# Kernel optimization log

Hardware: AMD Instinct MI355X
Metric: run time of the kernel (lower is better)

Reference implementation:

```python
import jax, jax.numpy as jnp
import numpy as np

D = 3          # matrix dimension (fixed in source)
WIDTH = 23     # hidden channel width (fixed in source)
B = 524288     # batch of 3x3 symmetric matrices

# layer channel dims: {1:1}->{1:W}, W->W, W->W, W->1
_LAYER_DIMS = [(1, WIDTH), (WIDTH, WIDTH), (WIDTH, WIDTH), (WIDTH, 1)]


def setup_inputs() -> dict:
    key = jax.random.key(0)
    ks = jax.random.split(key, 1 + 3 * len(_LAYER_DIMS))
    a = jax.random.normal(ks[0], (B, D, D), dtype=jnp.float32)
    x = a + jnp.swapaxes(a, -1, -2)  # symmetric inputs, as eigh expects
    inp = {"x": x}
    for li, (ic, oc) in enumerate(_LAYER_DIMS):
        s = 1.0 / np.sqrt(2.0 * ic * D)
        inp[f"w_id{li}"] = (jax.random.normal(ks[1 + 3 * li], (oc, ic)) * s).astype(jnp.float32)
        inp[f"w_sum{li}"] = (jax.random.normal(ks[2 + 3 * li], (oc, ic)) * s).astype(jnp.float32)
        inp[f"b{li}"] = jnp.zeros((oc,), dtype=jnp.float32)
    return inp


def _perm_layer(t, w_id, w_sum, b):
    # t: (B, in_c, D). S_D-equivariant linear map on order-1 tensors:
    # identity basis + all-ones(sum) basis + constant-vector bias.
    y = jnp.einsum('oc,bcd->bod', w_id, t)
    y = y + jnp.einsum('oc,bc->bo', w_sum, t.sum(-1))[:, :, None]
    return y + b[None, :, None]


def reference(x, w_id0, w_sum0, b0, w_id1, w_sum1, b1,
              w_id2, w_sum2, b2, w_id3, w_sum3, b3):
    evals, evecs = jnp.linalg.eigh(x)          # (B,D), (B,D,D)
    t = evals[:, None, :]                      # (B,1,D)
    layers = [(w_id0, w_sum0, b0), (w_id1, w_sum1, b1),
              (w_id2, w_sum2, b2), (w_id3, w_sum3, b3)]
    for i, (wi, ws, b) in enumerate(layers):
        t = _perm_layer(t, wi, ws, b)
        if i < len(layers) - 1:
            t = jax.nn.relu(t)
    ev = t[:, 0, :]                            # (B,D) transformed eigenvalues
    # eigvecs @ diag(ev) @ eigvecs^T, batched
    return jnp.einsum('bik,bk,bjk->bij', evecs, ev, evecs)
```

## Files before the change

kernel.cpp:

```cpp
#include <hip/hip_runtime.h>
#include <math.h>


#define MLP_W 23

typedef _Float16 h2    __attribute__((ext_vector_type(2)));
typedef _Float16 f16x4 __attribute__((ext_vector_type(4)));
typedef _Float16 f16x8 __attribute__((ext_vector_type(8)));
typedef float    f32x4 __attribute__((ext_vector_type(4)));
typedef float    v2f   __attribute__((ext_vector_type(2)));
typedef float    f4a   __attribute__((ext_vector_type(4), aligned(4)));

__device__ __attribute__((aligned(16))) h2 g_afrag[2][2][2][64][4];
__device__ __attribute__((aligned(16))) h2 g_a3frag[64][4];
__device__ __attribute__((aligned(16))) float g_l0[3][24];

__global__ void svh_prep_kernel(const float* __restrict__ wi0, const float* __restrict__ ws0,
                                const float* __restrict__ b0,
                                const float* __restrict__ wi1, const float* __restrict__ ws1,
                                const float* __restrict__ wi2, const float* __restrict__ ws2,
                                const float* __restrict__ wi3, const float* __restrict__ ws3) {
    int t = blockIdx.x * blockDim.x + threadIdx.x;
    if (t < 512) {
        int lane  = t & 63;
        int mt    = (t >> 6) & 1;
        int mat   = (t >> 7) & 1;
        int layer = (t >> 8) & 1;
        const float* W = layer ? (mat ? ws2 : wi2) : (mat ? ws1 : wi1);
        int row = mt * 16 + (lane & 15);
        int g   = lane >> 4;
#pragma unroll
        for (int dw = 0; dw < 4; ++dw) {
            int k0 = 8 * g + 2 * dw, k1 = k0 + 1;
            float a = (row < MLP_W && k0 < MLP_W) ? W[row * MLP_W + k0] : 0.0f;
            float b = (row < MLP_W && k1 < MLP_W) ? W[row * MLP_W + k1] : 0.0f;
            g_afrag[layer][mat][mt][lane][dw] = (h2){(_Float16)a, (_Float16)b};
        }
    }
    if (t < 64) {
        int lane = t;
        int row  = lane & 15;
        int g    = lane >> 4;
#pragma unroll
        for (int dw = 0; dw < 4; ++dw) {
            int k0 = 8 * g + 2 * dw, k1 = k0 + 1;
            float a = 0.0f, b = 0.0f;
            if (row == 0) {
                a = (k0 < MLP_W) ? wi3[k0] : 0.0f;
                b = (k1 < MLP_W) ? wi3[k1] : 0.0f;
            } else if (row == 1) {
                a = (k0 < MLP_W) ? ws3[k0] : 0.0f;
                b = (k1 < MLP_W) ? ws3[k1] : 0.0f;
            }
            g_a3frag[lane][dw] = (h2){(_Float16)a, (_Float16)b};
        }
    }
    if (t < 24) {
        g_l0[0][t] = (t < MLP_W) ? wi0[t] : 0.0f;
        g_l0[1][t] = (t < MLP_W) ? ws0[t] : 0.0f;
        g_l0[2][t] = (t < MLP_W) ? b0[t]  : 0.0f;
    }
}

__device__ __forceinline__ float sinv(float d) {
    return (fabsf(d) > 1e-20f) ? (1.0f / d) : 0.0f;
}

__device__ __forceinline__ f32x4 mm16(f16x8 a, f16x8 b) {
    return __builtin_amdgcn_mfma_f32_16x16x32_f16(a, b, (f32x4){0.f, 0.f, 0.f, 0.f}, 0, 0, 0);
}
__device__ __forceinline__ f32x4 mm16a(f16x8 a, f16x8 b, f32x4 c) {
    return __builtin_amdgcn_mfma_f32_16x16x32_f16(a, b, c, 0, 0, 0);
}

#define COLB 144
#define ZOFF (64 * COLB)
#define LDSZ (ZOFF + 16)

__global__ __launch_bounds__(64, 4)
void svh_eig_mlp_kernel(
    const float* __restrict__ x,
    const float* __restrict__ bb1, const float* __restrict__ bb2, const float* __restrict__ bb3,
    float* __restrict__ out, int B)
{
    __shared__ alignas(16) unsigned char lds[LDSZ];

    const int lane = threadIdx.x;
    const int g    = lane >> 4;
    const int c16  = lane & 15;
    int idx  = blockIdx.x * 64 + lane;
    int cidx = (idx < B) ? idx : (B - 1);

    const float* xp = x + (size_t)cidx * 9;
    f4a xa = *(const f4a*)(xp);
    f4a xb = *(const f4a*)(xp + 4);
    float x22 = xp[8];
    float x00 = xa[0], x01 = xa[1], x02 = xa[2];
    float x11 = xb[0], x12 = xb[1];

    if (lane == 0) *(f32x4*)(lds + ZOFF) = (f32x4){0.f, 0.f, 0.f, 0.f};

    float q   = (x00 + x11 + x22) * (1.0f / 3.0f);
    float a00 = x00 - q, a11 = x11 - q, a22 = x22 - q;
    float p1  = x01 * x01 + x02 * x02 + x12 * x12;
    float p2  = a00 * a00 + a11 * a11 + a22 * a22 + 2.0f * p1;
    float p   = sqrtf(p2 * (1.0f / 6.0f));
    float ip  = sinv(p);
    float d00 = a00 * ip, d11 = a11 * ip, d22 = a22 * ip;
    float c01 = x01 * ip, c02 = x02 * ip, c12 = x12 * ip;
    float detB = d00 * (d11 * d22 - c12 * c12)
               - c01 * (c01 * d22 - c12 * c02)
               + c02 * (c01 * c12 - d11 * c02);
    float r = 0.5f * detB;
    r = fminf(1.0f, fmaxf(-1.0f, r));
    float phi  = acosf(r) * (1.0f / 3.0f);
    float cph  = __cosf(phi);
    float sph  = sqrtf(fmaxf(0.0f, 1.0f - cph * cph));
    const float SQ3 = 1.7320508075688772f;
    float lc = q + 2.0f * p * cph;
    float la = q - p * cph - SQ3 * p * sph;
    float lb = q - p * cph + SQ3 * p * sph;

    {
        float S = la + lb + lc;
        v2f Sv = {S, S}, lav = {la, la}, lbv = {lb, lb}, lcv = {lc, lc};
        v2f z2 = {0.f, 0.f};
        const v2f* L0WI = (const v2f*)g_l0[0];
        const v2f* L0WS = (const v2f*)g_l0[1];
        const v2f* L0BB = (const v2f*)g_l0[2];
        const int base = lane * COLB;
#pragma unroll
        for (int m = 0; m < 6; ++m) {
            v2f wiA = L0WI[2 * m], wiB = L0WI[2 * m + 1];
            v2f uA  = __builtin_elementwise_fma(L0WS[2 * m],     Sv, L0BB[2 * m]);
            v2f uB  = __builtin_elementwise_fma(L0WS[2 * m + 1], Sv, L0BB[2 * m + 1]);
            v2f a0 = __builtin_elementwise_max(__builtin_elementwise_fma(wiA, lav, uA), z2);
            v2f b0 = __builtin_elementwise_max(__builtin_elementwise_fma(wiB, lav, uB), z2);
            v2f a1 = __builtin_elementwise_max(__builtin_elementwise_fma(wiA, lbv, uA), z2);
            v2f b1 = __builtin_elementwise_max(__builtin_elementwise_fma(wiB, lbv, uB), z2);
            v2f a2 = __builtin_elementwise_max(__builtin_elementwise_fma(wiA, lcv, uA), z2);
            v2f b2 = __builtin_elementwise_max(__builtin_elementwise_fma(wiB, lcv, uB), z2);
            int cb = base + (m >> 1) * 48 + (m & 1) * 8;
            *(f16x4*)(lds + cb +  0) = (f16x4){(_Float16)a0.x, (_Float16)a0.y, (_Float16)b0.x, (_Float16)b0.y};
            *(f16x4*)(lds + cb + 16) = (f16x4){(_Float16)a1.x, (_Float16)a1.y, (_Float16)b1.x, (_Float16)b1.y};
            *(f16x4*)(lds + cb + 32) = (f16x4){(_Float16)a2.x, (_Float16)a2.y, (_Float16)b2.x, (_Float16)b2.y};
        }
    }

    const f16x8 A3 = *(const f16x8*)(&g_a3frag[lane][0]);

    float eva = 0.0f, evb = 0.0f, evc = 0.0f;
    const f32x4 z4 = {0.f, 0.f, 0.f, 0.f};

#pragma unroll
    for (int L = 0; L < 2; ++L) {
        f16x8 WiM0 = *(const f16x8*)(&g_afrag[L][0][0][lane][0]);
        f16x8 WiM1 = *(const f16x8*)(&g_afrag[L][0][1][lane][0]);
        f16x8 WsM0 = *(const f16x8*)(&g_afrag[L][1][0][lane][0]);
        f16x8 WsM1 = *(const f16x8*)(&g_afrag[L][1][1][lane][0]);
        const float* bb = L ? bb2 : bb1;
        f32x4 bvec[2];
#pragma unroll
        for (int mt = 0; mt < 2; ++mt)
#pragma unroll
            for (int rr = 0; rr < 4; ++rr) {
                int row = mt * 16 + 4 * g + rr;
                bvec[mt][rr] = (row < MLP_W) ? bb[row] : 0.0f;
            }

#pragma unroll
        for (int pp = 0; pp < 4; ++pp) {
            const int colb = (16 * pp + c16) * COLB;
            f16x8 bf[3];
#pragma unroll
            for (int h = 0; h < 3; ++h) {
                int off = (g == 3) ? ZOFF : (colb + g * 48 + h * 16);
                bf[h] = *(const f16x8*)(lds + off);
            }
            f32x4 c0m0 = mm16(WiM0, bf[0]);
            f32x4 c0m1 = mm16(WiM1, bf[0]);
            f32x4 c1m0 = mm16(WiM0, bf[1]);
            f32x4 c1m1 = mm16(WiM1, bf[1]);
            f32x4 c2m0 = mm16(WiM0, bf[2]);
            f32x4 c2m1 = mm16(WiM1, bf[2]);
            f32x4 sm0 = mm16a(WsM0, bf[2], mm16a(WsM0, bf[1], mm16(WsM0, bf[0])));
            f32x4 sm1 = mm16a(WsM1, bf[2], mm16a(WsM1, bf[1], mm16(WsM1, bf[0])));

#pragma unroll
            for (int mt = 0; mt < 2; ++mt) {
                if (mt == 1 && g >= 2) continue;
                f32x4 c0 = (mt == 0) ? c0m0 : c0m1;
                f32x4 c1 = (mt == 0) ? c1m0 : c1m1;
                f32x4 c2 = (mt == 0) ? c2m0 : c2m1;
                f32x4 cs = (mt == 0) ? sm0  : sm1;
                f32x4 u  = cs + bvec[mt];
                f32x4 y0 = __builtin_elementwise_max(c0 + u, z4);
                f32x4 y1 = __builtin_elementwise_max(c1 + u, z4);
                f32x4 y2 = __builtin_elementwise_max(c2 + u, z4);
                int wb = colb + (2 * mt + (g >> 1)) * 48 + (g & 1) * 8;
                *(f16x4*)(lds + wb +  0) = (f16x4){(_Float16)y0[0], (_Float16)y0[1], (_Float16)y0[2], (_Float16)y0[3]};
                *(f16x4*)(lds + wb + 16) = (f16x4){(_Float16)y1[0], (_Float16)y1[1], (_Float16)y1[2], (_Float16)y1[3]};
                *(f16x4*)(lds + wb + 32) = (f16x4){(_Float16)y2[0], (_Float16)y2[1], (_Float16)y2[2], (_Float16)y2[3]};
            }

            if (L == 1) {
                f16x8 b2f[3];
#pragma unroll
                for (int h = 0; h < 3; ++h) {
                    int off = (g == 3) ? ZOFF : (colb + g * 48 + h * 16);
                    b2f[h] = *(const f16x8*)(lds + off);
                }
                f32x4 D0 = mm16(A3, b2f[0]);
                f32x4 D1 = mm16(A3, b2f[1]);
                f32x4 D2 = mm16(A3, b2f[2]);
                float ssum = D0[1] + D1[1] + D2[1];
                float ea = D0[0] + ssum;
                float eb = D1[0] + ssum;
                float ec = D2[0] + ssum;
                ea = __shfl(ea, c16);
                eb = __shfl(eb, c16);
                ec = __shfl(ec, c16);
                bool own = (g == pp);
                eva = own ? ea : eva;
                evb = own ? eb : evb;
                evc = own ? ec : evc;
            }
        }
    }

    {
        float b3v = bb3[0];
        eva += b3v; evb += b3v; evc += b3v;
    }

    float g1 = (evb - eva) * sinv(lb - la);
    float g2 = (evc - evb) * sinv(lc - lb);
    float c2 = (g2 - g1) * sinv(lc - la);

    float m100 = x00 - la, m111 = x11 - la, m122 = x22 - la;
    float m200 = x00 - lb, m211 = x11 - lb, m222 = x22 - lb;

    float P00 = m100 * m200 + x01 * x01 + x02 * x02;
    float P01 = m100 * x01 + x01 * m211 + x02 * x12;
    float P02 = m100 * x02 + x01 * x12 + x02 * m222;
    float P11 = x01 * x01 + m111 * m211 + x12 * x12;
    float P12 = x01 * x02 + m111 * x12 + x12 * m222;
    float P22 = x02 * x02 + x12 * x12 + m122 * m222;

    float o00 = fmaf(g1, m100, eva) + c2 * P00;
    float o01 = g1 * x01 + c2 * P01;
    float o02 = g1 * x02 + c2 * P02;
    float o11 = fmaf(g1, m111, eva) + c2 * P11;
    float o12 = g1 * x12 + c2 * P12;
    float o22 = fmaf(g1, m122, eva) + c2 * P22;

    if (idx < B) {
        float* op = out + (size_t)idx * 9;
        op[0] = o00; op[1] = o01; op[2] = o02;
        op[3] = o01; op[4] = o11; op[5] = o12;
        op[6] = o02; op[7] = o12; op[8] = o22;
    }
}

extern "C" void kernel_launch(void* const* d_in, const int* in_sizes, int n_in,
                              void* d_out, int out_size, void* d_ws, size_t ws_size,
                              hipStream_t stream) {
    const float* x   = (const float*)d_in[0];
    const float* wi0 = (const float*)d_in[1];
    const float* ws0 = (const float*)d_in[2];
    const float* b0  = (const float*)d_in[3];
    const float* wi1 = (const float*)d_in[4];
    const float* ws1 = (const float*)d_in[5];
    const float* b1  = (const float*)d_in[6];
    const float* wi2 = (const float*)d_in[7];
    const float* ws2 = (const float*)d_in[8];
    const float* b2  = (const float*)d_in[9];
    const float* wi3 = (const float*)d_in[10];
    const float* ws3 = (const float*)d_in[11];
    const float* b3  = (const float*)d_in[12];

    int B = in_sizes[0] / 9;
    float* out = (float*)d_out;

    {
        dim3 block(256);
        dim3 grid(2);
        hipLaunchKernelGGL(svh_prep_kernel, grid, block, 0, stream,
                           wi0, ws0, b0, wi1, ws1, wi2, ws2, wi3, ws3);
    }

    dim3 block(64);
    dim3 grid((B + 63) / 64);
    hipLaunchKernelGGL(svh_eig_mlp_kernel, grid, block, 0, stream,
                       x, b1, b2, b3, out, B);
}
```

Before: 117.0 us.

## Fold layer biases into MFMA via ones channel, polynomial acos, vector stores

Folds the hidden-layer biases into the padded 24th input channel of the sum-weight fragments by setting that channel to 1 in the activations. This removes per-thread bias loads and adds. Also replaces acosf with a short minimax polynomial times a square root, and writes the output with two 16-byte-vector stores plus one scalar store instead of nine scalar stores. The bias now passes through fp16, which may cost some accuracy, and the polynomial acos is less precise.

```diff
diff --git a/kernel.cpp b/kernel.cpp
--- a/kernel.cpp
+++ b/kernel.cpp
@@ -18,7 +18,9 @@
 __global__ void svh_prep_kernel(const float* __restrict__ wi0, const float* __restrict__ ws0,
                                 const float* __restrict__ b0,
                                 const float* __restrict__ wi1, const float* __restrict__ ws1,
+                                const float* __restrict__ b1,
                                 const float* __restrict__ wi2, const float* __restrict__ ws2,
+                                const float* __restrict__ b2,
                                 const float* __restrict__ wi3, const float* __restrict__ ws3) {
     int t = blockIdx.x * blockDim.x + threadIdx.x;
     if (t < 512) {
@@ -26,7 +28,8 @@
         int mt    = (t >> 6) & 1;
         int mat   = (t >> 7) & 1;
         int layer = (t >> 8) & 1;
-        const float* W = layer ? (mat ? ws2 : wi2) : (mat ? ws1 : wi1);
+        const float* W  = layer ? (mat ? ws2 : wi2) : (mat ? ws1 : wi1);
+        const float* BI = layer ? b2 : b1;
         int row = mt * 16 + (lane & 15);
         int g   = lane >> 4;
 #pragma unroll
@@ -34,6 +37,7 @@
             int k0 = 8 * g + 2 * dw, k1 = k0 + 1;
             float a = (row < MLP_W && k0 < MLP_W) ? W[row * MLP_W + k0] : 0.0f;
             float b = (row < MLP_W && k1 < MLP_W) ? W[row * MLP_W + k1] : 0.0f;
+            if (mat == 1 && k1 == 23 && row < MLP_W) b = BI[row];
             g_afrag[layer][mat][mt][lane][dw] = (h2){(_Float16)a, (_Float16)b};
         }
     }
@@ -80,7 +84,7 @@
 __global__ __launch_bounds__(64, 4)
 void svh_eig_mlp_kernel(
     const float* __restrict__ x,
-    const float* __restrict__ bb1, const float* __restrict__ bb2, const float* __restrict__ bb3,
+    const float* __restrict__ bb3,
     float* __restrict__ out, int B)
 {
     __shared__ alignas(16) unsigned char lds[LDSZ];
@@ -113,7 +117,18 @@
                + c02 * (c01 * c12 - d11 * c02);
     float r = 0.5f * detB;
     r = fminf(1.0f, fmaxf(-1.0f, r));
-    float phi  = acosf(r) * (1.0f / 3.0f);
+    float ar  = fabsf(r);
+    float sq  = sqrtf(fmaxf(0.0f, 1.0f - ar));
+    float po  = fmaf(ar, -0.0012624911f, 0.0066700901f);
+    po = fmaf(ar, po, -0.0170881256f);
+    po = fmaf(ar, po,  0.0308918810f);
+    po = fmaf(ar, po, -0.0501743046f);
+    po = fmaf(ar, po,  0.0889789874f);
+    po = fmaf(ar, po, -0.2145988016f);
+    po = fmaf(ar, po,  1.5707963050f);
+    float acs = sq * po * (1.0f / 3.0f);
+    const float PI3 = 1.0471975511965976f;
+    float phi = (r >= 0.0f) ? acs : (PI3 - acs);
     float cph  = __cosf(phi);
     float sph  = sqrtf(fmaxf(0.0f, 1.0f - cph * cph));
     const float SQ3 = 1.7320508075688772f;
@@ -140,6 +155,7 @@
             v2f b1 = __builtin_elementwise_max(__builtin_elementwise_fma(wiB, lbv, uB), z2);
             v2f a2 = __builtin_elementwise_max(__builtin_elementwise_fma(wiA, lcv, uA), z2);
             v2f b2 = __builtin_elementwise_max(__builtin_elementwise_fma(wiB, lcv, uB), z2);
+            if (m == 5) b0.y = 1.0f;
             int cb = base + (m >> 1) * 48 + (m & 1) * 8;
             *(f16x4*)(lds + cb +  0) = (f16x4){(_Float16)a0.x, (_Float16)a0.y, (_Float16)b0.x, (_Float16)b0.y};
             *(f16x4*)(lds + cb + 16) = (f16x4){(_Float16)a1.x, (_Float16)a1.y, (_Float16)b1.x, (_Float16)b1.y};
@@ -158,15 +174,6 @@
         f16x8 WiM1 = *(const f16x8*)(&g_afrag[L][0][1][lane][0]);
         f16x8 WsM0 = *(const f16x8*)(&g_afrag[L][1][0][lane][0]);
         f16x8 WsM1 = *(const f16x8*)(&g_afrag[L][1][1][lane][0]);
-        const float* bb = L ? bb2 : bb1;
-        f32x4 bvec[2];
-#pragma unroll
-        for (int mt = 0; mt < 2; ++mt)
-#pragma unroll
-            for (int rr = 0; rr < 4; ++rr) {
-                int row = mt * 16 + 4 * g + rr;
-                bvec[mt][rr] = (row < MLP_W) ? bb[row] : 0.0f;
-            }
 
 #pragma unroll
         for (int pp = 0; pp < 4; ++pp) {
@@ -192,11 +199,11 @@
                 f32x4 c0 = (mt == 0) ? c0m0 : c0m1;
                 f32x4 c1 = (mt == 0) ? c1m0 : c1m1;
                 f32x4 c2 = (mt == 0) ? c2m0 : c2m1;
-                f32x4 cs = (mt == 0) ? sm0  : sm1;
-                f32x4 u  = cs + bvec[mt];
+                f32x4 u  = (mt == 0) ? sm0  : sm1;
                 f32x4 y0 = __builtin_elementwise_max(c0 + u, z4);
                 f32x4 y1 = __builtin_elementwise_max(c1 + u, z4);
                 f32x4 y2 = __builtin_elementwise_max(c2 + u, z4);
+                if (mt == 1 && g == 1) y0[3] = 1.0f;
                 int wb = colb + (2 * mt + (g >> 1)) * 48 + (g & 1) * 8;
                 *(f16x4*)(lds + wb +  0) = (f16x4){(_Float16)y0[0], (_Float16)y0[1], (_Float16)y0[2], (_Float16)y0[3]};
                 *(f16x4*)(lds + wb + 16) = (f16x4){(_Float16)y1[0], (_Float16)y1[1], (_Float16)y1[2], (_Float16)y1[3]};
@@ -256,9 +263,11 @@
 
     if (idx < B) {
         float* op = out + (size_t)idx * 9;
-        op[0] = o00; op[1] = o01; op[2] = o02;
-        op[3] = o01; op[4] = o11; op[5] = o12;
-        op[6] = o02; op[7] = o12; op[8] = o22;
+        f4a s0v = {o00, o01, o02, o01};
+        f4a s1v = {o11, o12, o02, o12};
+        *(f4a*)(op)     = s0v;
+        *(f4a*)(op + 4) = s1v;
+        op[8] = o22;
     }
 }
 
@@ -286,11 +295,11 @@
         dim3 block(256);
         dim3 grid(2);
         hipLaunchKernelGGL(svh_prep_kernel, grid, block, 0, stream,
-                           wi0, ws0, b0, wi1, ws1, wi2, ws2, wi3, ws3);
+                           wi0, ws0, b0, wi1, ws1, b1, wi2, ws2, b2, wi3, ws3);
     }
 
     dim3 block(64);
     dim3 grid((B + 63) / 64);
     hipLaunchKernelGGL(svh_eig_mlp_kernel, grid, block, 0, stream,
-                       x, b1, b2, b3, out, B);
-}
+                       x, b3, out, B);
+}
```

Result: no change. 119.1 us (+1.8%).
